# Optimization experiments

Hardware: AMD Instinct MI355X
Metric: run time of the kernel (lower is better)

The kernel has to match this reference:

```python
import jax, jax.numpy as jnp
import numpy as np

B, LF, LS, C = 4, 256, 128, 8
D = 8            # d_embed
D_STATE = 16
D_CONV = 4
DI = 2 * D       # d_inner = expand * d_model
DT_RANK = 1      # ceil(d_model / 16)
EPS = 1e-5


def setup_inputs() -> dict:
    key = jax.random.key(0)
    ks = jax.random.split(key, 14)
    n = lambda k, shp, s=0.1: jax.random.normal(k, shp, jnp.float32) * s
    return {
        "x": jax.random.normal(ks[0], (B, LF, LS, C), jnp.float32),
        "lift_w": n(ks[1], (C, D), 1.0),
        "lift_b": n(ks[2], (C, D)),
        "in_proj_w": n(ks[3], (C, 2 * DI, D), 0.3),
        "conv_w": n(ks[4], (C, DI, D_CONV), 0.3),
        "conv_b": n(ks[5], (C, DI)),
        "x_proj_w": n(ks[6], (C, DT_RANK + 2 * D_STATE, DI), 0.3),
        "dt_w": n(ks[7], (C, DI, DT_RANK), 0.3),
        "dt_b": n(ks[8], (C, DI), 0.5) - 2.0,  # softplus -> small positive dt
        "A_log": jnp.tile(jnp.log(jnp.arange(1, D_STATE + 1, dtype=jnp.float32)), (C, DI, 1)),
        "D_skip": jnp.ones((C, DI), jnp.float32),
        "out_w": n(ks[9], (C, D, DI), 0.3),
        "blk_w": n(ks[10], (C, D, D), 0.3),
        "blk_b": n(ks[11], (C, D)),
        "ln_g": jnp.ones((C * D,), jnp.float32),
        "ln_b": jnp.zeros((C * D,), jnp.float32),
    }


def _mamba_channel(params, zc):
    """One per-channel Mamba block. zc: (N, Lf, D) -> pooled (N, D)."""
    ipw, cw, cb, xpw, dtw, dtb, Alog, Dsk, ow, bw, bb = params
    N, Lf, _ = zc.shape
    xz = zc @ ipw.T                                   # (N, Lf, 2*DI)
    x_in, zg = xz[..., :DI], xz[..., DI:]
    # causal depthwise conv over time (kernel D_CONV, left-padded)
    xp = jnp.pad(x_in, ((0, 0), (D_CONV - 1, 0), (0, 0)))
    x_conv = cb
    for k in range(D_CONV):
        x_conv = x_conv + xp[:, k:k + Lf, :] * cw[:, k]
    x_conv = jax.nn.silu(x_conv)                      # (N, Lf, DI)
    x_dbl = x_conv @ xpw.T                            # (N, Lf, DT_RANK+2*DS)
    dt_lo = x_dbl[..., :DT_RANK]
    Bm = x_dbl[..., DT_RANK:DT_RANK + D_STATE]        # (N, Lf, DS)
    Cm = x_dbl[..., DT_RANK + D_STATE:]               # (N, Lf, DS)
    dt = jax.nn.softplus(dt_lo @ dtw.T + dtb)         # (N, Lf, DI)
    A = -jnp.exp(Alog)                                # (DI, DS)

    def step(h, inp):
        dt_t, B_t, C_t, x_t = inp                     # (N,DI),(N,DS),(N,DS),(N,DI)
        dA = jnp.exp(dt_t[..., None] * A)             # (N, DI, DS)
        h = dA * h + (dt_t * x_t)[..., None] * B_t[:, None, :]
        y = jnp.einsum('nds,ns->nd', h, C_t)
        return h, y

    h0 = jnp.zeros((N, DI, D_STATE), zc.dtype)
    xs = (dt.transpose(1, 0, 2), Bm.transpose(1, 0, 2),
          Cm.transpose(1, 0, 2), x_conv.transpose(1, 0, 2))
    _, ys = jax.lax.scan(step, h0, xs)                # (Lf, N, DI)
    y = ys.transpose(1, 0, 2) + Dsk * x_conv          # (N, Lf, DI)
    y = y * jax.nn.silu(zg)
    out = y @ ow.T                                    # (N, Lf, D) inner Mamba out_proj
    blk = jax.nn.silu(out @ bw.T + bb)                # MambaSSMBlock out_proj + silu
    return blk.mean(axis=1)                           # pool over Lf -> (N, D)


def _forward(x, lift_w, lift_b, in_proj_w, conv_w, conv_b, x_proj_w, dt_w, dt_b,
             A_log, D_skip, out_w, blk_w, blk_b, ln_g, ln_b):
    Bb, Lf, Ls, Cc = x.shape
    xw = x.transpose(0, 2, 3, 1).reshape(Bb * Ls, Cc, Lf)       # (N, C, Lf)
    # grouped 1x1 conv lift: (N, C, Lf, D)
    z = xw[..., None] * lift_w[None, :, None, :] + lift_b[None, :, None, :]
    z = z.transpose(1, 0, 2, 3)                                 # (C, N, Lf, D)
    params = (in_proj_w, conv_w, conv_b, x_proj_w, dt_w, dt_b,
              A_log, D_skip, out_w, blk_w, blk_b)
    pooled = jax.vmap(_mamba_channel)(params, z)                # (C, N, D)
    feat = pooled.transpose(1, 0, 2).reshape(Bb, Ls, Cc * D)    # concat channels
    mu = feat.mean(-1, keepdims=True)
    var = feat.var(-1, keepdims=True)
    return (feat - mu) / jnp.sqrt(var + EPS) * ln_g + ln_b


def reference(x, lift_w, lift_b, in_proj_w, conv_w, conv_b, x_proj_w, dt_w, dt_b,
              A_log, D_skip, out_w, blk_w, blk_b, ln_g, ln_b):
    return _forward(x, lift_w, lift_b, in_proj_w, conv_w, conv_b, x_proj_w,
                    dt_w, dt_b, A_log, D_skip, out_w, blk_w, blk_b, ln_g, ln_b)
```

## Files before the change

kernel.cpp:

```cpp
#include <hip/hip_runtime.h>

#define LOG2E 1.4426950408889634f
#define LN2   0.6931471805599453f

typedef float v2f __attribute__((ext_vector_type(2)));
typedef short bf16x8 __attribute__((ext_vector_type(8)));
typedef float f32x4  __attribute__((ext_vector_type(4)));

#define MW   0
#define FRQ  128
#define SWTOT 1152

#define ABC  0
#define ADW  576
#define AY0  1152
#define AY1  1440
#define AXV  1728
#define AWORDS 1748

#define MEMFENCE() asm volatile("" ::: "memory")

__device__ __forceinline__ float fexp2(float x){ return __builtin_amdgcn_exp2f(x); }
__device__ __forceinline__ float flog2(float x){ return __builtin_amdgcn_logf(x); }
__device__ __forceinline__ float frcp (float x){ return __builtin_amdgcn_rcpf(x); }
__device__ __forceinline__ float siluf(float x){ return x * frcp(1.0f + fexp2(-x * LOG2E)); }
__device__ __forceinline__ float softplusf(float x){
  float r = flog2(1.0f + fexp2(x * LOG2E)) * LN2;
  return x > 15.0f ? x : r;
}
__device__ __forceinline__ unsigned int bf16rtn(float x){
  unsigned int u = __float_as_uint(x);
  return (u + (0x7FFFu + ((u >> 16) & 1u))) & 0xFFFF0000u;
}

__global__ __launch_bounds__(128, 4) void mamba_k(
    const float* __restrict__ xg,   const float* __restrict__ lwg,  const float* __restrict__ lbg,
    const float* __restrict__ ipwg, const float* __restrict__ cwg,  const float* __restrict__ cbg,
    const float* __restrict__ xpwg, const float* __restrict__ dtwg, const float* __restrict__ dtbg,
    const float* __restrict__ alogg,const float* __restrict__ dskg, const float* __restrict__ owg,
    const float* __restrict__ bwg,  const float* __restrict__ bbg,  float* __restrict__ feat)
{
  __shared__ __align__(16) float s_w [SWTOT];
  __shared__ __align__(16) float s_ar[2*AWORDS];

  const int tid  = threadIdx.x;
  const int wid  = tid >> 6;
  const int lane = tid & 63;
  const int c    = blockIdx.x & 7;
  const int n    = (blockIdx.x >> 3)*2 + wid;
  const int t4   = lane >> 2;
  const int q    = lane & 3;
  const int tm   = lane & 15;
  const int gm   = lane >> 4;
  const int addrA = (tm*4 + (gm & 1)*2) * 4;
  const int addrB = addrA + 4;

  float* AR = s_ar + wid*AWORDS;
  const float* xpc = xpwg + c*528;

  {
    int d = tid >> 4, i = tid & 15;
    float m = 0.f;
    #pragma unroll
    for (int k = 0; k < 8; ++k) m += bwg[c*64 + d*8 + k] * owg[c*128 + k*16 + i];
    s_w[MW + tid] = m;
  }
  for (int i = tid; i < 1024; i += 128) {
    int f  = i >> 8, l = (i >> 2) & 63, jj = i & 3;
    int H  = f & 1, isF2 = f >> 1;
    const float* wr = xpc + (1 + 16*H + (l & 15))*16;
    int k0 = 8*(l >> 4) + 2*jj;
    unsigned int d = 0;
    #pragma unroll
    for (int e = 0; e < 2; ++e) {
      int k = k0 + e;
      float w = wr[k & 15];
      unsigned int hi = bf16rtn(w);
      unsigned int v;
      if (k < 16)     v = hi;
      else if (isF2)  v = 0u;
      else            v = bf16rtn(w - __uint_as_float(hi));
      d |= (v >> 16) << (16*e);
    }
    s_w[FRQ + i] = __uint_as_float(d);
  }
  if (lane < 3) AR[AXV + lane] = 0.f;

  const float4 xpr0 = *(const float4*)(xpc + q*4);

  float Px[4], Qx[4], Pz[4], Qz[4], cwr[4][4], af[4], dtwr[4], dtbr[4], dskr[4];
  #pragma unroll
  for (int j = 0; j < 4; ++j) {
    const int i = q*4 + j;
    float px=0.f, qx=0.f, pz=0.f, qz=0.f;
    #pragma unroll
    for (int d = 0; d < 8; ++d) {
      float wx = ipwg[c*256 + i*8 + d];
      float wz = ipwg[c*256 + (16+i)*8 + d];
      float lw = lwg[c*8+d], lb = lbg[c*8+d];
      px += wx*lw; qx += wx*lb;
      pz += wz*lw; qz += wz*lb;
    }
    Px[j]=px; Qx[j]=qx; Pz[j]=pz; Qz[j]=qz;
    float sw = 0.f;
    #pragma unroll
    for (int k = 0; k < 4; ++k) { cwr[j][k] = cwg[c*64 + i*4 + k]; sw += cwr[j][k]; }
    af[j]   = cbg[c*16+i] + qx*sw;
    dtwr[j] = dtwg[c*16+i];
    dtbr[j] = dtbg[c*16+i];
    dskr[j] = dskg[c*16+i];
  }
  const float bbr0 = bbg[c*8 + q*2 + 0];
  const float bbr1 = bbg[c*8 + q*2 + 1];

  float Am0, dAm;
  {
    const int ab = c*256 + t4*16 + q*4;
    Am0 = -fexp2(alogg[ab+0] * LOG2E) * LOG2E;
    float Am1 = -fexp2(alogg[ab+1] * LOG2E) * LOG2E;
    dAm = Am1 - Am0;
  }
  __syncthreads();

  float* bcB = AR + ABC + tm*36 + gm*4;
  float* bcC = bcB + 16;

  v2f h01 = {0.f, 0.f}, h23 = {0.f, 0.f};
  float pacc0 = 0.f, pacc1 = 0.f;
  float xca[4], xcb[4];

  const int xbase = (n>>7)*262144 + (n&127)*8 + c;
  float xcur_a = xg[xbase + t4*1024];
  float xcur_b = xg[xbase + (16 + t4)*1024];

  #pragma unroll 1
  for (int s = 0; s < 8; ++s) {
    float xnxt_a = xg[xbase + ((((s+1)&7)*32      ) + t4)*1024];
    float xnxt_b = xg[xbase + ((((s+1)&7)*32 + 16 ) + t4)*1024];

    #pragma unroll 1
    for (int half = 0; half < 2; ++half) {
      const float xcur = half ? xcur_b : xcur_a;
      float* xc = half ? xcb : xca;
      float* AY = AR + (half ? AY1 : AY0);

      if (s > 0 || half > 0) {
        MEMFENCE();
        if (lane < 3) AR[AXV + lane] = AR[AXV + 16 + lane];
      }
      if (q == 0) AR[AXV + 3 + t4] = xcur;
      MEMFENCE();
      {
        float x0 = AR[AXV + t4], x1 = AR[AXV + t4 + 1],
              x2 = AR[AXV + t4 + 2], x3 = AR[AXV + t4 + 3];
        #pragma unroll
        for (int j = 0; j < 4; ++j) {
          float u = cwr[j][0]*x0 + cwr[j][1]*x1 + cwr[j][2]*x2 + cwr[j][3]*x3;
          float v = af[j] + Px[j]*u;
          if (s == 0 && half == 0 && t4 < 3) {
            float cs = cwr[j][0];
            if (t4 < 2) cs += cwr[j][1];
            if (t4 < 1) cs += cwr[j][2];
            v -= Qx[j]*cs;
          }
          xc[j] = siluf(v);
        }
        unsigned int h0 = bf16rtn(xc[0]), h1 = bf16rtn(xc[1]),
                     h2 = bf16rtn(xc[2]), h3 = bf16rtn(xc[3]);
        unsigned int l0 = bf16rtn(xc[0] - __uint_as_float(h0));
        unsigned int l1 = bf16rtn(xc[1] - __uint_as_float(h1));
        unsigned int l2 = bf16rtn(xc[2] - __uint_as_float(h2));
        unsigned int l3 = bf16rtn(xc[3] - __uint_as_float(h3));
        unsigned int P0 = (h0 >> 16) | h1, P1 = (h2 >> 16) | h3;
        unsigned int L0 = (l0 >> 16) | l1, L1 = (l2 >> 16) | l3;
        union BF { unsigned int u[4]; bf16x8 h; } BH, BL;
        BH.u[0] = (unsigned int)__builtin_amdgcn_ds_bpermute(addrA, (int)P0);
        BH.u[1] = (unsigned int)__builtin_amdgcn_ds_bpermute(addrA, (int)P1);
        BH.u[2] = (unsigned int)__builtin_amdgcn_ds_bpermute(addrB, (int)P0);
        BH.u[3] = (unsigned int)__builtin_amdgcn_ds_bpermute(addrB, (int)P1);
        BL.u[0] = (unsigned int)__builtin_amdgcn_ds_bpermute(addrA, (int)L0);
        BL.u[1] = (unsigned int)__builtin_amdgcn_ds_bpermute(addrA, (int)L1);
        BL.u[2] = (unsigned int)__builtin_amdgcn_ds_bpermute(addrB, (int)L0);
        BL.u[3] = (unsigned int)__builtin_amdgcn_ds_bpermute(addrB, (int)L1);
        float dtlo;
        {
          v2f a = (v2f){xc[0], xc[1]} * (v2f){xpr0.x, xpr0.y};
          a    += (v2f){xc[2], xc[3]} * (v2f){xpr0.z, xpr0.w};
          float p = a.x + a.y;
          p += __shfl_xor(p, 1);
          p += __shfl_xor(p, 2);
          dtlo = p;
        }
        union AF { float4 f; bf16x8 h; } A10, A11, A20, A21;
        A10.f = *(const float4*)(s_w + FRQ +       lane*4);
        A11.f = *(const float4*)(s_w + FRQ + 256 + lane*4);
        A20.f = *(const float4*)(s_w + FRQ + 512 + lane*4);
        A21.f = *(const float4*)(s_w + FRQ + 768 + lane*4);
        f32x4 zz = {0.f, 0.f, 0.f, 0.f};
        f32x4 d0 = __builtin_amdgcn_mfma_f32_16x16x32_bf16(A20.h, BL.h, zz, 0, 0, 0);
        d0       = __builtin_amdgcn_mfma_f32_16x16x32_bf16(A10.h, BH.h, d0, 0, 0, 0);
        f32x4 d1 = __builtin_amdgcn_mfma_f32_16x16x32_bf16(A21.h, BL.h, zz, 0, 0, 0);
        d1       = __builtin_amdgcn_mfma_f32_16x16x32_bf16(A11.h, BH.h, d1, 0, 0, 0);
        *(float4*)bcB = make_float4(d0[0], d0[1], d0[2], d0[3]);
        *(float4*)bcC = make_float4(d1[0], d1[1], d1[2], d1[3]);
        {
          float dd0 = softplusf(dtlo*dtwr[0]+dtbr[0]);
          float dd1 = softplusf(dtlo*dtwr[1]+dtbr[1]);
          float dd2 = softplusf(dtlo*dtwr[2]+dtbr[2]);
          float dd3 = softplusf(dtlo*dtwr[3]+dtbr[3]);
          float* dwp = AR + ADW + t4*2;
          *(float2*)(dwp + (q*4+0)*36) = make_float2(dd0, dd0*xc[0]);
          *(float2*)(dwp + (q*4+1)*36) = make_float2(dd1, dd1*xc[1]);
          *(float2*)(dwp + (q*4+2)*36) = make_float2(dd2, dd2*xc[2]);
          *(float2*)(dwp + (q*4+3)*36) = make_float2(dd3, dd3*xc[3]);
        }
      }
      MEMFENCE();
      {
        const float* pB = AR + ABC + q*4;
        const float* pC = AR + ABC + 16 + q*4;
        const float* pd = AR + ADW + t4*36;
        float* py = AY + t4*18;
        #pragma unroll 2
        for (int tp = 0; tp < 8; ++tp) {
          float4 dwp = *(const float4*)(pd + tp*4);
          float ylast;
          {
            float4 bv = *(const float4*)(pB + (2*tp)*36);
            float4 cv = *(const float4*)(pC + (2*tp)*36);
            float e0 = fexp2(dwp.x*Am0);
            float r  = fexp2(dwp.x*dAm);
            float r2 = r*r;
            v2f e01 = (v2f){e0, e0*r};
            v2f e23 = e01 * r2;
            h01 = h01*e01 + (v2f){bv.x, bv.y} * dwp.y;
            h23 = h23*e23 + (v2f){bv.z, bv.w} * dwp.y;
            v2f t = h01 * (v2f){cv.x, cv.y};
            t    += h23 * (v2f){cv.z, cv.w};
            float yp = t.x + t.y;
            yp += __shfl_xor(yp, 1);
            yp += __shfl_xor(yp, 2);
            ylast = yp;
          }
          {
            float4 bv = *(const float4*)(pB + (2*tp+1)*36);
            float4 cv = *(const float4*)(pC + (2*tp+1)*36);
            float e0 = fexp2(dwp.z*Am0);
            float r  = fexp2(dwp.z*dAm);
            float r2 = r*r;
            v2f e01 = (v2f){e0, e0*r};
            v2f e23 = e01 * r2;
            h01 = h01*e01 + (v2f){bv.x, bv.y} * dwp.w;
            h23 = h23*e23 + (v2f){bv.z, bv.w} * dwp.w;
            v2f t = h01 * (v2f){cv.x, cv.y};
            t    += h23 * (v2f){cv.z, cv.w};
            float yp = t.x + t.y;
            yp += __shfl_xor(yp, 1);
            yp += __shfl_xor(yp, 2);
            if (q == 0) *(float2*)(py + 2*tp) = make_float2(ylast, yp);
          }
        }
      }
      MEMFENCE();
    }
    {
      v2f yfa01, yfa23, yfb01, yfb23;
      {
        float ya[4], yb[4];
        #pragma unroll
        for (int j = 0; j < 4; ++j) {
          ya[j] = AR[AY0 + (q*4+j)*18 + t4];
          yb[j] = AR[AY1 + (q*4+j)*18 + t4];
        }
        float fa[4], fb[4];
        #pragma unroll
        for (int j = 0; j < 4; ++j) {
          float ga = siluf(xcur_a*Pz[j] + Qz[j]);
          float gb = siluf(xcur_b*Pz[j] + Qz[j]);
          fa[j] = (ya[j] + dskr[j]*xca[j]) * ga;
          fb[j] = (yb[j] + dskr[j]*xcb[j]) * gb;
        }
        yfa01 = (v2f){fa[0], fa[1]}; yfa23 = (v2f){fa[2], fa[3]};
        yfb01 = (v2f){fb[0], fb[1]}; yfb23 = (v2f){fb[2], fb[3]};
      }
      float ova[8], ovb[8];
      #pragma unroll
      for (int d = 0; d < 8; ++d) {
        const float* wr = s_w + MW + d*16 + q*4;
        float4 w = *(const float4*)(wr);
        v2f aa = yfa01 * (v2f){w.x, w.y};
        aa    += yfa23 * (v2f){w.z, w.w};
        v2f ab = yfb01 * (v2f){w.x, w.y};
        ab    += yfb23 * (v2f){w.z, w.w};
        float sa = aa.x + aa.y;
        float sb = ab.x + ab.y;
        sa += __shfl_xor(sa, 1); sa += __shfl_xor(sa, 2);
        sb += __shfl_xor(sb, 1); sb += __shfl_xor(sb, 2);
        ova[d] = sa; ovb[d] = sb;
      }
      {
        float a0 = (q&2) ? ((q&1) ? ova[6] : ova[4]) : ((q&1) ? ova[2] : ova[0]);
        float a1 = (q&2) ? ((q&1) ? ova[7] : ova[5]) : ((q&1) ? ova[3] : ova[1]);
        float b0 = (q&2) ? ((q&1) ? ovb[6] : ovb[4]) : ((q&1) ? ovb[2] : ovb[0]);
        float b1 = (q&2) ? ((q&1) ? ovb[7] : ovb[5]) : ((q&1) ? ovb[3] : ovb[1]);
        pacc0 += siluf(bbr0 + a0) + siluf(bbr0 + b0);
        pacc1 += siluf(bbr1 + a1) + siluf(bbr1 + b1);
      }
    }
    xcur_a = xnxt_a;
    xcur_b = xnxt_b;
  }

  #pragma unroll
  for (int m = 4; m < 64; m <<= 1) {
    pacc0 += __shfl_xor(pacc0, m);
    pacc1 += __shfl_xor(pacc1, m);
  }
  if (t4 == 0) {
    feat[n*64 + c*8 + q*2 + 0] = pacc0 * (1.0f/256.0f);
    feat[n*64 + c*8 + q*2 + 1] = pacc1 * (1.0f/256.0f);
  }
}

__global__ __launch_bounds__(256) void ln_k(const float* __restrict__ feat,
    const float* __restrict__ g, const float* __restrict__ b, float* __restrict__ out)
{
  const int row = blockIdx.x*4 + (threadIdx.x >> 6);
  const int l = threadIdx.x & 63;
  float v = feat[row*64 + l];
  float s = v, qq = v*v;
  #pragma unroll
  for (int m = 1; m < 64; m <<= 1) { s += __shfl_xor(s, m); qq += __shfl_xor(qq, m); }
  float mu  = s * (1.0f/64.0f);
  float var = qq * (1.0f/64.0f) - mu*mu;
  float rs  = __builtin_amdgcn_rsqf(var + 1e-5f);
  out[row*64 + l] = (v - mu) * rs * g[l] + b[l];
}

extern "C" void kernel_launch(void* const* d_in, const int* in_sizes, int n_in,
                              void* d_out, int out_size, void* d_ws, size_t ws_size,
                              hipStream_t stream)
{
  const float* xg    = (const float*)d_in[0];
  const float* lwg   = (const float*)d_in[1];
  const float* lbg   = (const float*)d_in[2];
  const float* ipwg  = (const float*)d_in[3];
  const float* cwg   = (const float*)d_in[4];
  const float* cbg   = (const float*)d_in[5];
  const float* xpwg  = (const float*)d_in[6];
  const float* dtwg  = (const float*)d_in[7];
  const float* dtbg  = (const float*)d_in[8];
  const float* alogg = (const float*)d_in[9];
  const float* dskg  = (const float*)d_in[10];
  const float* owg   = (const float*)d_in[11];
  const float* bwg   = (const float*)d_in[12];
  const float* bbg   = (const float*)d_in[13];
  const float* lng   = (const float*)d_in[14];
  const float* lnb   = (const float*)d_in[15];
  float* feat = (float*)d_ws;

  mamba_k<<<dim3(2048), dim3(128), 0, stream>>>(xg, lwg, lbg, ipwg, cwg, cbg, xpwg,
                                                dtwg, dtbg, alogg, dskg, owg, bwg, bbg, feat);
  ln_k<<<dim3(128), dim3(256), 0, stream>>>(feat, lng, lnb, (float*)d_out);
}
```

Baseline: 189.8 us.

## Overlap second half-chunk conv/MFMA with first half-chunk scan; drop extra weight tiles

The two half-chunks per step are software-pipelined. The conv, SiLU and MFMA projection for the second half now run before the selective scan of the first half, and their results are committed to LDS only after that scan. This is meant to hide MFMA and bpermute latency behind the serial scan. Separately, the hi-only weight fragments are dropped and the hi+lo fragments are reused for the x-lo product. That shrinks shared memory and removes two LDS loads per half, but adds a small w_lo*x_lo term that slightly changes rounding.

```diff
diff --git a/kernel.cpp b/kernel.cpp
--- a/kernel.cpp
+++ b/kernel.cpp
@@ -9,7 +9,7 @@
 
 #define MW   0
 #define FRQ  128
-#define SWTOT 1152
+#define SWTOT 640
 
 #define ABC  0
 #define ADW  576
@@ -65,9 +65,8 @@
     for (int k = 0; k < 8; ++k) m += bwg[c*64 + d*8 + k] * owg[c*128 + k*16 + i];
     s_w[MW + tid] = m;
   }
-  for (int i = tid; i < 1024; i += 128) {
-    int f  = i >> 8, l = (i >> 2) & 63, jj = i & 3;
-    int H  = f & 1, isF2 = f >> 1;
+  for (int i = tid; i < 512; i += 128) {
+    int H = i >> 8, l = (i >> 2) & 63, jj = i & 3;
     const float* wr = xpc + (1 + 16*H + (l & 15))*16;
     int k0 = 8*(l >> 4) + 2*jj;
     unsigned int d = 0;
@@ -76,10 +75,7 @@
       int k = k0 + e;
       float w = wr[k & 15];
       unsigned int hi = bf16rtn(w);
-      unsigned int v;
-      if (k < 16)     v = hi;
-      else if (isF2)  v = 0u;
-      else            v = bf16rtn(w - __uint_as_float(hi));
+      unsigned int v = (k < 16) ? hi : bf16rtn(w - __uint_as_float(hi));
       d |= (v >> 16) << (16*e);
     }
     s_w[FRQ + i] = __uint_as_float(d);
@@ -133,136 +129,142 @@
   float xcur_a = xg[xbase + t4*1024];
   float xcur_b = xg[xbase + (16 + t4)*1024];
 
+  auto a2_compute = [&](float* xc, bool boundary, f32x4& d0, f32x4& d1, float& dtlo){
+    float x0 = AR[AXV + t4], x1 = AR[AXV + t4 + 1],
+          x2 = AR[AXV + t4 + 2], x3 = AR[AXV + t4 + 3];
+    #pragma unroll
+    for (int j = 0; j < 4; ++j) {
+      float u = cwr[j][0]*x0 + cwr[j][1]*x1 + cwr[j][2]*x2 + cwr[j][3]*x3;
+      float v = af[j] + Px[j]*u;
+      if (boundary && t4 < 3) {
+        float cs = cwr[j][0];
+        if (t4 < 2) cs += cwr[j][1];
+        if (t4 < 1) cs += cwr[j][2];
+        v -= Qx[j]*cs;
+      }
+      xc[j] = siluf(v);
+    }
+    unsigned int h0 = bf16rtn(xc[0]), h1 = bf16rtn(xc[1]),
+                 h2v = bf16rtn(xc[2]), h3 = bf16rtn(xc[3]);
+    unsigned int l0 = bf16rtn(xc[0] - __uint_as_float(h0));
+    unsigned int l1 = bf16rtn(xc[1] - __uint_as_float(h1));
+    unsigned int l2 = bf16rtn(xc[2] - __uint_as_float(h2v));
+    unsigned int l3 = bf16rtn(xc[3] - __uint_as_float(h3));
+    unsigned int P0 = (h0 >> 16) | h1, P1 = (h2v >> 16) | h3;
+    unsigned int L0 = (l0 >> 16) | l1, L1 = (l2 >> 16) | l3;
+    union BF { unsigned int u[4]; bf16x8 h; } BH, BL;
+    BH.u[0] = (unsigned int)__builtin_amdgcn_ds_bpermute(addrA, (int)P0);
+    BH.u[1] = (unsigned int)__builtin_amdgcn_ds_bpermute(addrA, (int)P1);
+    BH.u[2] = (unsigned int)__builtin_amdgcn_ds_bpermute(addrB, (int)P0);
+    BH.u[3] = (unsigned int)__builtin_amdgcn_ds_bpermute(addrB, (int)P1);
+    BL.u[0] = (unsigned int)__builtin_amdgcn_ds_bpermute(addrA, (int)L0);
+    BL.u[1] = (unsigned int)__builtin_amdgcn_ds_bpermute(addrA, (int)L1);
+    BL.u[2] = (unsigned int)__builtin_amdgcn_ds_bpermute(addrB, (int)L0);
+    BL.u[3] = (unsigned int)__builtin_amdgcn_ds_bpermute(addrB, (int)L1);
+    {
+      v2f a = (v2f){xc[0], xc[1]} * (v2f){xpr0.x, xpr0.y};
+      a    += (v2f){xc[2], xc[3]} * (v2f){xpr0.z, xpr0.w};
+      float p = a.x + a.y;
+      p += __shfl_xor(p, 1);
+      p += __shfl_xor(p, 2);
+      dtlo = p;
+    }
+    union AF { float4 f; bf16x8 h; } A10, A11;
+    A10.f = *(const float4*)(s_w + FRQ +       lane*4);
+    A11.f = *(const float4*)(s_w + FRQ + 256 + lane*4);
+    f32x4 zz = {0.f, 0.f, 0.f, 0.f};
+    d0 = __builtin_amdgcn_mfma_f32_16x16x32_bf16(A10.h, BL.h, zz, 0, 0, 0);
+    d0 = __builtin_amdgcn_mfma_f32_16x16x32_bf16(A10.h, BH.h, d0, 0, 0, 0);
+    d1 = __builtin_amdgcn_mfma_f32_16x16x32_bf16(A11.h, BL.h, zz, 0, 0, 0);
+    d1 = __builtin_amdgcn_mfma_f32_16x16x32_bf16(A11.h, BH.h, d1, 0, 0, 0);
+  };
+
+  auto commit = [&](const f32x4& d0, const f32x4& d1, float dtlo, const float* xc){
+    *(float4*)bcB = make_float4(d0[0], d0[1], d0[2], d0[3]);
+    *(float4*)bcC = make_float4(d1[0], d1[1], d1[2], d1[3]);
+    float dd0 = softplusf(dtlo*dtwr[0]+dtbr[0]);
+    float dd1 = softplusf(dtlo*dtwr[1]+dtbr[1]);
+    float dd2 = softplusf(dtlo*dtwr[2]+dtbr[2]);
+    float dd3 = softplusf(dtlo*dtwr[3]+dtbr[3]);
+    float* dwp = AR + ADW + t4*2;
+    *(float2*)(dwp + (q*4+0)*36) = make_float2(dd0, dd0*xc[0]);
+    *(float2*)(dwp + (q*4+1)*36) = make_float2(dd1, dd1*xc[1]);
+    *(float2*)(dwp + (q*4+2)*36) = make_float2(dd2, dd2*xc[2]);
+    *(float2*)(dwp + (q*4+3)*36) = make_float2(dd3, dd3*xc[3]);
+  };
+
+  auto scan = [&](float* AY){
+    const float* pB = AR + ABC + q*4;
+    const float* pC = AR + ABC + 16 + q*4;
+    const float* pd = AR + ADW + t4*36;
+    float* py = AY + t4*18;
+    #pragma unroll 2
+    for (int tp = 0; tp < 8; ++tp) {
+      float4 dwp = *(const float4*)(pd + tp*4);
+      float ylast;
+      {
+        float4 bv = *(const float4*)(pB + (2*tp)*36);
+        float4 cv = *(const float4*)(pC + (2*tp)*36);
+        float e0 = fexp2(dwp.x*Am0);
+        float r  = fexp2(dwp.x*dAm);
+        float r2 = r*r;
+        v2f e01 = (v2f){e0, e0*r};
+        v2f e23 = e01 * r2;
+        h01 = h01*e01 + (v2f){bv.x, bv.y} * dwp.y;
+        h23 = h23*e23 + (v2f){bv.z, bv.w} * dwp.y;
+        v2f t = h01 * (v2f){cv.x, cv.y};
+        t    += h23 * (v2f){cv.z, cv.w};
+        float yp = t.x + t.y;
+        yp += __shfl_xor(yp, 1);
+        yp += __shfl_xor(yp, 2);
+        ylast = yp;
+      }
+      {
+        float4 bv = *(const float4*)(pB + (2*tp+1)*36);
+        float4 cv = *(const float4*)(pC + (2*tp+1)*36);
+        float e0 = fexp2(dwp.z*Am0);
+        float r  = fexp2(dwp.z*dAm);
+        float r2 = r*r;
+        v2f e01 = (v2f){e0, e0*r};
+        v2f e23 = e01 * r2;
+        h01 = h01*e01 + (v2f){bv.x, bv.y} * dwp.w;
+        h23 = h23*e23 + (v2f){bv.z, bv.w} * dwp.w;
+        v2f t = h01 * (v2f){cv.x, cv.y};
+        t    += h23 * (v2f){cv.z, cv.w};
+        float yp = t.x + t.y;
+        yp += __shfl_xor(yp, 1);
+        yp += __shfl_xor(yp, 2);
+        if (q == 0) *(float2*)(py + 2*tp) = make_float2(ylast, yp);
+      }
+    }
+  };
+
   #pragma unroll 1
   for (int s = 0; s < 8; ++s) {
     float xnxt_a = xg[xbase + ((((s+1)&7)*32      ) + t4)*1024];
     float xnxt_b = xg[xbase + ((((s+1)&7)*32 + 16 ) + t4)*1024];
 
-    #pragma unroll 1
-    for (int half = 0; half < 2; ++half) {
-      const float xcur = half ? xcur_b : xcur_a;
-      float* xc = half ? xcb : xca;
-      float* AY = AR + (half ? AY1 : AY0);
-
-      if (s > 0 || half > 0) {
-        MEMFENCE();
-        if (lane < 3) AR[AXV + lane] = AR[AXV + 16 + lane];
-      }
-      if (q == 0) AR[AXV + 3 + t4] = xcur;
+    if (s > 0) {
       MEMFENCE();
-      {
-        float x0 = AR[AXV + t4], x1 = AR[AXV + t4 + 1],
-              x2 = AR[AXV + t4 + 2], x3 = AR[AXV + t4 + 3];
-        #pragma unroll
-        for (int j = 0; j < 4; ++j) {
-          float u = cwr[j][0]*x0 + cwr[j][1]*x1 + cwr[j][2]*x2 + cwr[j][3]*x3;
-          float v = af[j] + Px[j]*u;
-          if (s == 0 && half == 0 && t4 < 3) {
-            float cs = cwr[j][0];
-            if (t4 < 2) cs += cwr[j][1];
-            if (t4 < 1) cs += cwr[j][2];
-            v -= Qx[j]*cs;
-          }
-          xc[j] = siluf(v);
-        }
-        unsigned int h0 = bf16rtn(xc[0]), h1 = bf16rtn(xc[1]),
-                     h2 = bf16rtn(xc[2]), h3 = bf16rtn(xc[3]);
-        unsigned int l0 = bf16rtn(xc[0] - __uint_as_float(h0));
-        unsigned int l1 = bf16rtn(xc[1] - __uint_as_float(h1));
-        unsigned int l2 = bf16rtn(xc[2] - __uint_as_float(h2));
-        unsigned int l3 = bf16rtn(xc[3] - __uint_as_float(h3));
-        unsigned int P0 = (h0 >> 16) | h1, P1 = (h2 >> 16) | h3;
-        unsigned int L0 = (l0 >> 16) | l1, L1 = (l2 >> 16) | l3;
-        union BF { unsigned int u[4]; bf16x8 h; } BH, BL;
-        BH.u[0] = (unsigned int)__builtin_amdgcn_ds_bpermute(addrA, (int)P0);
-        BH.u[1] = (unsigned int)__builtin_amdgcn_ds_bpermute(addrA, (int)P1);
-        BH.u[2] = (unsigned int)__builtin_amdgcn_ds_bpermute(addrB, (int)P0);
-        BH.u[3] = (unsigned int)__builtin_amdgcn_ds_bpermute(addrB, (int)P1);
-        BL.u[0] = (unsigned int)__builtin_amdgcn_ds_bpermute(addrA, (int)L0);
-        BL.u[1] = (unsigned int)__builtin_amdgcn_ds_bpermute(addrA, (int)L1);
-        BL.u[2] = (unsigned int)__builtin_amdgcn_ds_bpermute(addrB, (int)L0);
-        BL.u[3] = (unsigned int)__builtin_amdgcn_ds_bpermute(addrB, (int)L1);
-        float dtlo;
-        {
-          v2f a = (v2f){xc[0], xc[1]} * (v2f){xpr0.x, xpr0.y};
-          a    += (v2f){xc[2], xc[3]} * (v2f){xpr0.z, xpr0.w};
-          float p = a.x + a.y;
-          p += __shfl_xor(p, 1);
-          p += __shfl_xor(p, 2);
-          dtlo = p;
-        }
-        union AF { float4 f; bf16x8 h; } A10, A11, A20, A21;
-        A10.f = *(const float4*)(s_w + FRQ +       lane*4);
-        A11.f = *(const float4*)(s_w + FRQ + 256 + lane*4);
-        A20.f = *(const float4*)(s_w + FRQ + 512 + lane*4);
-        A21.f = *(const float4*)(s_w + FRQ + 768 + lane*4);
-        f32x4 zz = {0.f, 0.f, 0.f, 0.f};
-        f32x4 d0 = __builtin_amdgcn_mfma_f32_16x16x32_bf16(A20.h, BL.h, zz, 0, 0, 0);
-        d0       = __builtin_amdgcn_mfma_f32_16x16x32_bf16(A10.h, BH.h, d0, 0, 0, 0);
-        f32x4 d1 = __builtin_amdgcn_mfma_f32_16x16x32_bf16(A21.h, BL.h, zz, 0, 0, 0);
-        d1       = __builtin_amdgcn_mfma_f32_16x16x32_bf16(A11.h, BH.h, d1, 0, 0, 0);
-        *(float4*)bcB = make_float4(d0[0], d0[1], d0[2], d0[3]);
-        *(float4*)bcC = make_float4(d1[0], d1[1], d1[2], d1[3]);
-        {
-          float dd0 = softplusf(dtlo*dtwr[0]+dtbr[0]);
-          float dd1 = softplusf(dtlo*dtwr[1]+dtbr[1]);
-          float dd2 = softplusf(dtlo*dtwr[2]+dtbr[2]);
-          float dd3 = softplusf(dtlo*dtwr[3]+dtbr[3]);
-          float* dwp = AR + ADW + t4*2;
-          *(float2*)(dwp + (q*4+0)*36) = make_float2(dd0, dd0*xc[0]);
-          *(float2*)(dwp + (q*4+1)*36) = make_float2(dd1, dd1*xc[1]);
-          *(float2*)(dwp + (q*4+2)*36) = make_float2(dd2, dd2*xc[2]);
-          *(float2*)(dwp + (q*4+3)*36) = make_float2(dd3, dd3*xc[3]);
-        }
-      }
-      MEMFENCE();
-      {
-        const float* pB = AR + ABC + q*4;
-        const float* pC = AR + ABC + 16 + q*4;
-        const float* pd = AR + ADW + t4*36;
-        float* py = AY + t4*18;
-        #pragma unroll 2
-        for (int tp = 0; tp < 8; ++tp) {
-          float4 dwp = *(const float4*)(pd + tp*4);
-          float ylast;
-          {
-            float4 bv = *(const float4*)(pB + (2*tp)*36);
-            float4 cv = *(const float4*)(pC + (2*tp)*36);
-            float e0 = fexp2(dwp.x*Am0);
-            float r  = fexp2(dwp.x*dAm);
-            float r2 = r*r;
-            v2f e01 = (v2f){e0, e0*r};
-            v2f e23 = e01 * r2;
-            h01 = h01*e01 + (v2f){bv.x, bv.y} * dwp.y;
-            h23 = h23*e23 + (v2f){bv.z, bv.w} * dwp.y;
-            v2f t = h01 * (v2f){cv.x, cv.y};
-            t    += h23 * (v2f){cv.z, cv.w};
-            float yp = t.x + t.y;
-            yp += __shfl_xor(yp, 1);
-            yp += __shfl_xor(yp, 2);
-            ylast = yp;
-          }
-          {
-            float4 bv = *(const float4*)(pB + (2*tp+1)*36);
-            float4 cv = *(const float4*)(pC + (2*tp+1)*36);
-            float e0 = fexp2(dwp.z*Am0);
-            float r  = fexp2(dwp.z*dAm);
-            float r2 = r*r;
-            v2f e01 = (v2f){e0, e0*r};
-            v2f e23 = e01 * r2;
-            h01 = h01*e01 + (v2f){bv.x, bv.y} * dwp.w;
-            h23 = h23*e23 + (v2f){bv.z, bv.w} * dwp.w;
-            v2f t = h01 * (v2f){cv.x, cv.y};
-            t    += h23 * (v2f){cv.z, cv.w};
-            float yp = t.x + t.y;
-            yp += __shfl_xor(yp, 1);
-            yp += __shfl_xor(yp, 2);
-            if (q == 0) *(float2*)(py + 2*tp) = make_float2(ylast, yp);
-          }
-        }
-      }
-      MEMFENCE();
-    }
+      if (lane < 3) AR[AXV + lane] = AR[AXV + 16 + lane];
+    }
+    if (q == 0) AR[AXV + 3 + t4] = xcur_a;
+    MEMFENCE();
+    f32x4 d0a, d1a; float dtloa;
+    a2_compute(xca, s == 0, d0a, d1a, dtloa);
+    commit(d0a, d1a, dtloa, xca);
+    MEMFENCE();
+    if (lane < 3) AR[AXV + lane] = AR[AXV + 16 + lane];
+    if (q == 0) AR[AXV + 3 + t4] = xcur_b;
+    MEMFENCE();
+    f32x4 d0b, d1b; float dtlob;
+    a2_compute(xcb, false, d0b, d1b, dtlob);
+    scan(AR + AY0);
+    MEMFENCE();
+    commit(d0b, d1b, dtlob, xcb);
+    MEMFENCE();
+    scan(AR + AY1);
+    MEMFENCE();
     {
       v2f yfa01, yfa23, yfb01, yfb23;
       {
```

Measured after the change: 183.8 us. 1.03x faster.
